# Kernel tuning notes

Hardware: AMD Instinct MI355X
Metric: run time of the kernel (lower is better)

The kernel has to match this reference:

```python
import jax, jax.numpy as jnp
import numpy as np

MAXDISP = 48
GROUP = 8
EPS = 1e-5


def setup_inputs() -> dict:
    key = jax.random.key(0)
    k1, k2 = jax.random.split(key)
    x = jax.random.normal(k1, (2, 64, 96, 320), dtype=jnp.float32)
    y = jax.random.normal(k2, (2, 64, 96, 320), dtype=jnp.float32)
    return {"x": x, "y": y}


def reference(x, y):
    # Faithful translation of CostVolume.forward.
    # torch's unfold over left-zero-padded y at kernel position d picks
    # y_pad[..., j + d]; per-window L2 norm over channels reduces to a
    # per-pixel channel norm (padded zeros normalize to zero), so we
    # normalize once and gather shifted columns.
    D = MAXDISP + 1
    b, c, h, w = x.shape
    cpg = c // GROUP
    xg = x.reshape(b, GROUP, cpg, h, w)
    yg = y.reshape(b, GROUP, cpg, h, w)
    xn = xg / (jnp.linalg.norm(xg, axis=2, keepdims=True) + EPS)
    yn = yg / (jnp.linalg.norm(yg, axis=2, keepdims=True) + EPS)
    # left zero-pad width dim by MAXDISP (padded zeros stay zero after norm)
    y_pad = jnp.pad(yn, ((0, 0), (0, 0), (0, 0), (0, 0), (MAXDISP, 0)))
    # after torch.flip on the disparity axis, disparity k compares x[:, j]
    # with y[:, j - k]  ->  padded index j + MAXDISP - k
    idx = jnp.arange(w)[None, :] + MAXDISP - jnp.arange(D)[:, None]  # [D, w]
    y_shift = y_pad[..., idx]  # [b, g, cpg, h, D, w]
    cost = jnp.sum(jnp.abs(xn[:, :, :, :, None, :] - y_shift), axis=2)  # [b,g,h,D,w]
    return jnp.transpose(cost, (0, 1, 3, 2, 4))  # [b, group, D, h, w]
```

## Files before the change

### kernel.cpp

```cpp
#include <hip/hip_runtime.h>


#define MAXDISP 48
#define NDISP   49
#define HH      96
#define WW      320
#define HW      (HH * WW)
#define EPSN    1e-5f

__global__ __launch_bounds__(320, 4) void cost_volume_kernel(
    const float* __restrict__ x, const float* __restrict__ y,
    float* __restrict__ out)
{
    __shared__ float4 ylds[2][2][WW / 2];

    const int tid   = threadIdx.x;
    const int q     = tid % 160;
    const int r     = tid / 160;
    const int j     = 2 * q;
    const int dbase = 24 * r;

    const int blk = blockIdx.x;
    const int h   = blk % HH;
    const int bg  = blk / HH;

    const int inBase = bg * 8 * HW + h * WW + j;

    float xa[8], xb[8];
    float xsa = 0.f, xsb = 0.f;
#pragma unroll
    for (int cc = 0; cc < 8; ++cc) {
        const float2 xi = *reinterpret_cast<const float2*>(x + inBase + cc * HW);
        xa[cc] = xi.x; xb[cc] = xi.y;
        xsa += xi.x * xi.x; xsb += xi.y * xi.y;
    }
    const float xia = 1.f / (sqrtf(xsa) + EPSN);
    const float xib = 1.f / (sqrtf(xsb) + EPSN);
    float sAbsA = 0.f, sAbsB = 0.f;
#pragma unroll
    for (int cc = 0; cc < 8; ++cc) {
        xa[cc] *= xia; xb[cc] *= xib;
        sAbsA += fabsf(xa[cc]);
        sAbsB += fabsf(xb[cc]);
    }

    if (tid < 160) {
        float ya[8], yb[8];
        float ysa = 0.f, ysb = 0.f;
#pragma unroll
        for (int cc = 0; cc < 8; ++cc) {
            const float2 yi = *reinterpret_cast<const float2*>(y + inBase + cc * HW);
            ya[cc] = yi.x; yb[cc] = yi.y;
            ysa += yi.x * yi.x; ysb += yi.y * yi.y;
        }
        const float yia = 1.f / (sqrtf(ysa) + EPSN);
        const float yib = 1.f / (sqrtf(ysb) + EPSN);
#pragma unroll
        for (int cc = 0; cc < 8; ++cc) { ya[cc] *= yia; yb[cc] *= yib; }
        ylds[0][0][q] = make_float4(ya[0], ya[1], ya[2], ya[3]);
        ylds[0][1][q] = make_float4(ya[4], ya[5], ya[6], ya[7]);
        ylds[1][0][q] = make_float4(yb[0], yb[1], yb[2], yb[3]);
        ylds[1][1][q] = make_float4(yb[4], yb[5], yb[6], yb[7]);
    }
    __syncthreads();

    const float4* const ldsE = &ylds[0][0][0];
    const float4* const ldsO = &ylds[1][0][0];

    const int p0  = j - dbase;
    const int ix0 = (p0 > 0 ? p0 : 0) >> 1;
    float4 yp0 = ldsE[ix0], yp1 = ldsE[160 + ix0];
    float4 yc0 = ldsO[ix0], yc1 = ldsO[160 + ix0];

    float* const outBase = out + bg * (NDISP * HW) + h * WW + j;

#define CV_STEP(D, FB, DO_FRESH)                                            \
    {                                                                       \
        float c0 = fabsf(xa[0] - yp0.x) + fabsf(xa[1] - yp0.y)              \
                 + fabsf(xa[2] - yp0.z) + fabsf(xa[3] - yp0.w)              \
                 + fabsf(xa[4] - yp1.x) + fabsf(xa[5] - yp1.y)              \
                 + fabsf(xa[6] - yp1.z) + fabsf(xa[7] - yp1.w);             \
        float c1 = fabsf(xb[0] - yc0.x) + fabsf(xb[1] - yc0.y)              \
                 + fabsf(xb[2] - yc0.z) + fabsf(xb[3] - yc0.w)              \
                 + fabsf(xb[4] - yc1.x) + fabsf(xb[5] - yc1.y)              \
                 + fabsf(xb[6] - yc1.z) + fabsf(xb[7] - yc1.w);             \
        c0 = ((D) <= j)     ? c0 : sAbsA;                                   \
        c1 = ((D) <= j + 1) ? c1 : sAbsB;                                   \
        *reinterpret_cast<float2*>(outBase + (D) * HW) = make_float2(c0, c1);\
        yc0 = yp0; yc1 = yp1;                                               \
        if (DO_FRESH) {                                                     \
            const int pn = j - (D) - 1;                                     \
            const int ix = (pn > 0 ? pn : 0) >> 1;                          \
            yp0 = (FB)[ix]; yp1 = (FB)[160 + ix];                           \
        }                                                                   \
    }

#pragma unroll
    for (int ii = 0; ii < 12; ++ii) {
        const int d0 = dbase + 2 * ii;
        CV_STEP(d0,     ldsO, 1);
        CV_STEP(d0 + 1, ldsE, 1);
    }
    CV_STEP(dbase + 24, ldsO, 0);

#undef CV_STEP
}

extern "C" void kernel_launch(void* const* d_in, const int* in_sizes, int n_in,
                              void* d_out, int out_size, void* d_ws, size_t ws_size,
                              hipStream_t stream) {
    const float* x = (const float*)d_in[0];
    const float* y = (const float*)d_in[1];
    float* out = (float*)d_out;
    dim3 grid(2 * 8 * HH);
    dim3 block(WW);
    cost_volume_kernel<<<grid, block, 0, stream>>>(x, y, out);
}
```

Baseline: 128.5 us.

## Process six rows per block with one thread per column pair over all disparities

Result: faster. 124.8 us, median of 2 (-2.9%).

```diff
diff --git a/kernel.cpp b/kernel.cpp
--- a/kernel.cpp
+++ b/kernel.cpp
@@ -7,22 +7,23 @@
 #define WW      320
 #define HW      (HH * WW)
 #define EPSN    1e-5f
+#define GROWS   6
 
-__global__ __launch_bounds__(320, 4) void cost_volume_kernel(
+__global__ __launch_bounds__(960, 4) void cost_volume_kernel(
     const float* __restrict__ x, const float* __restrict__ y,
     float* __restrict__ out)
 {
-    __shared__ float4 ylds[2][2][WW / 2];
+    __shared__ float4 ylds[GROWS][2][2][WW / 2];
 
-    const int tid   = threadIdx.x;
-    const int q     = tid % 160;
-    const int r     = tid / 160;
-    const int j     = 2 * q;
-    const int dbase = 24 * r;
+    const int tid = threadIdx.x;
+    const int q   = tid % 160;
+    const int r   = tid / 160;
+    const int j   = 2 * q;
 
     const int blk = blockIdx.x;
-    const int h   = blk % HH;
-    const int bg  = blk / HH;
+    const int hb  = blk % 16;
+    const int bg  = blk / 16;
+    const int h   = hb * GROWS + r;
 
     const int inBase = bg * 8 * HW + h * WW + j;
 
@@ -44,7 +45,7 @@
         sAbsB += fabsf(xb[cc]);
     }
 
-    if (tid < 160) {
+    {
         float ya[8], yb[8];
         float ysa = 0.f, ysb = 0.f;
 #pragma unroll
@@ -57,20 +58,18 @@
         const float yib = 1.f / (sqrtf(ysb) + EPSN);
 #pragma unroll
         for (int cc = 0; cc < 8; ++cc) { ya[cc] *= yia; yb[cc] *= yib; }
-        ylds[0][0][q] = make_float4(ya[0], ya[1], ya[2], ya[3]);
-        ylds[0][1][q] = make_float4(ya[4], ya[5], ya[6], ya[7]);
-        ylds[1][0][q] = make_float4(yb[0], yb[1], yb[2], yb[3]);
-        ylds[1][1][q] = make_float4(yb[4], yb[5], yb[6], yb[7]);
+        ylds[r][0][0][q] = make_float4(ya[0], ya[1], ya[2], ya[3]);
+        ylds[r][0][1][q] = make_float4(ya[4], ya[5], ya[6], ya[7]);
+        ylds[r][1][0][q] = make_float4(yb[0], yb[1], yb[2], yb[3]);
+        ylds[r][1][1][q] = make_float4(yb[4], yb[5], yb[6], yb[7]);
     }
     __syncthreads();
 
-    const float4* const ldsE = &ylds[0][0][0];
-    const float4* const ldsO = &ylds[1][0][0];
+    const float4* const ldsE = &ylds[r][0][0][0];
+    const float4* const ldsO = &ylds[r][1][0][0];
 
-    const int p0  = j - dbase;
-    const int ix0 = (p0 > 0 ? p0 : 0) >> 1;
-    float4 yp0 = ldsE[ix0], yp1 = ldsE[160 + ix0];
-    float4 yc0 = ldsO[ix0], yc1 = ldsO[160 + ix0];
+    float4 yp0 = ldsE[q], yp1 = ldsE[160 + q];
+    float4 yc0 = ldsO[q], yc1 = ldsO[160 + q];
 
     float* const outBase = out + bg * (NDISP * HW) + h * WW + j;
 
@@ -96,12 +95,12 @@
     }
 
 #pragma unroll
-    for (int ii = 0; ii < 12; ++ii) {
-        const int d0 = dbase + 2 * ii;
+    for (int ii = 0; ii < 24; ++ii) {
+        const int d0 = 2 * ii;
         CV_STEP(d0,     ldsO, 1);
         CV_STEP(d0 + 1, ldsE, 1);
     }
-    CV_STEP(dbase + 24, ldsO, 0);
+    CV_STEP(MAXDISP, ldsO, 0);
 
 #undef CV_STEP
 }
@@ -112,7 +111,7 @@
     const float* x = (const float*)d_in[0];
     const float* y = (const float*)d_in[1];
     float* out = (float*)d_out;
-    dim3 grid(2 * 8 * HH);
-    dim3 block(WW);
+    dim3 grid(16 * (HH / GROWS));
+    dim3 block(GROWS * (WW / 2));
     cost_volume_kernel<<<grid, block, 0, stream>>>(x, y, out);
 }
```
